# Optimization experiments

Measured on AMD Instinct MI355X. Metric: run time of the kernel, lower is better.

The kernel has to match this reference:

```python
import jax, jax.numpy as jnp
from jax import lax
import numpy as np

N, K, QK, W = 10, 10, 150, 128
D = 256
HID = 100
CHANS = [1, 16, 32, 64, 128, 256]
STRIDES = [2, 2, 1, 1, 1]
ITERS = 3
BN_EPS = 1e-5


def setup_inputs() -> dict:
    key = jax.random.key(0)
    ks = jax.random.split(key, 12)
    inp = {
        "support": jax.random.normal(ks[0], (N, K, 1, W, W), jnp.float32),
        "query": jax.random.normal(ks[1], (QK, 1, W, W), jnp.float32),
    }
    for i in range(5):
        inp[f"conv_w{i}"] = jax.random.normal(ks[2 + i], (CHANS[i + 1], CHANS[i], 3, 3), jnp.float32) * 0.05
        inp[f"bn_g{i}"] = jnp.ones((CHANS[i + 1],), jnp.float32)
        inp[f"bn_b{i}"] = jnp.zeros((CHANS[i + 1],), jnp.float32)
    inp["trans_w"] = jax.random.normal(ks[8], (D, D), jnp.float32) * 0.05
    inp["trans_b"] = jnp.zeros((D,), jnp.float32)
    inp["bil_w"] = jax.random.normal(ks[9], (HID, D, D), jnp.float32) * 0.02
    inp["score_w"] = jax.random.normal(ks[10], (1, HID), jnp.float32) * 0.1
    inp["score_b"] = jnp.zeros((1,), jnp.float32)
    return inp


def _block(x, w, g, b, s):
    # Conv2d(k=3, pad=1, stride=s, no bias) -> BatchNorm(eval: mean=0, var=1) -> ReLU -> MaxPool2d(2)
    x = lax.conv_general_dilated(x, w, (s, s), ((1, 1), (1, 1)),
                                 dimension_numbers=('NCHW', 'OIHW', 'NCHW'))
    scale = (g / jnp.sqrt(1.0 + BN_EPS))[None, :, None, None]
    x = jax.nn.relu(x * scale + b[None, :, None, None])
    return lax.reduce_window(x, -jnp.inf, lax.max, (1, 1, 2, 2), (1, 1, 2, 2), 'VALID')


def reference(support, query,
              conv_w0, conv_w1, conv_w2, conv_w3, conv_w4,
              bn_g0, bn_g1, bn_g2, bn_g3, bn_g4,
              bn_b0, bn_b1, bn_b2, bn_b3, bn_b4,
              trans_w, trans_b, bil_w, score_w, score_b):
    n, k = support.shape[0], support.shape[1]
    qk = query.shape[0]
    w = support.shape[3]

    ws = [conv_w0, conv_w1, conv_w2, conv_w3, conv_w4]
    gs = [bn_g0, bn_g1, bn_g2, bn_g3, bn_g4]
    bs = [bn_b0, bn_b1, bn_b2, bn_b3, bn_b4]

    # run the conv backbone on support+query jointly (BN is per-sample in eval mode)
    x = jnp.concatenate([support.reshape(n * k, 1, w, w), query], axis=0)
    for cw, g, b, s in zip(ws, gs, bs, STRIDES):
        x = _block(x, cw, g, b, s)
    feats = x.reshape(x.shape[0], -1)              # (n*k + qk, 256); spatial is 1x1
    sup = feats[:n * k].reshape(n, k, -1)          # (n, k, d)
    q = feats[n * k:]                              # (qk, d)

    # dynamic routing: Transformer(e) is recomputed each iter on the same input -> hoist
    e = sup @ trans_w.T + trans_b                  # (n, k, d)
    b0 = jnp.zeros((n, k), sup.dtype)

    def step(bb, _):
        dcoef = jax.nn.softmax(bb, axis=1)[:, :, None]   # (n, k, 1)
        c = (dcoef * e).sum(axis=1)                      # (n, d)
        cn = jnp.sqrt((c * c).sum(axis=1, keepdims=True))
        c = c * (cn / (cn * cn + 1.0))                   # squash: ||c||^2/(||c||^2+1)/||c||
        db = (c[:, None, :] * e).sum(axis=2)             # (n, k)
        return bb + db, c

    _, cs = lax.scan(step, b0, None, length=ITERS)
    proto = cs[-1]                                  # (n, d)

    # NTN: bilinear score for every (query, proto) pair, exploiting the pair structure
    t1 = jnp.einsum('nc,hce->nhe', proto, bil_w)    # (n, HID, d)
    v = jnp.einsum('nhe,qe->qnh', t1, q)            # (qk, n, HID)
    s = jax.nn.relu(v) @ score_w[0] + score_b[0]    # (qk, n)
    return jax.nn.log_softmax(s, axis=1)
```

## Files before the change

kernel.cpp:

```cpp
#include <hip/hip_runtime.h>
#include <math.h>


#define BN_SCALE rsqrtf(1.0f + 1e-5f)

#define OFF_A0    0
#define OFF_FEATS 4096000
#define OFF_E     4160000
#define OFF_PROTO 4185600
#define OFF_T1    4188160
#define OFF_W1T   4444160
#define OFF_W2T   4448768
#define OFF_W3T   4467200
#define OFF_W4T   4540928
#define OFF_TWT   4835840

__global__ void k_block0(const float* __restrict__ sup, const float* __restrict__ qry,
                         const float* __restrict__ w0, const float* __restrict__ g0,
                         const float* __restrict__ b0,
                         const float* __restrict__ w1, const float* __restrict__ w2,
                         const float* __restrict__ w3, const float* __restrict__ w4,
                         const float* __restrict__ tw, float* __restrict__ ws) {
  __shared__ float simg[33 * 132];
  float* a0  = ws + OFF_A0;
  float* w1t = ws + OFF_W1T;
  float* w2t = ws + OFF_W2T;
  float* w3t = ws + OFF_W3T;
  float* w4t = ws + OFF_W4T;
  float* twt = ws + OFF_TWT;
  float* t1  = ws + OFF_T1;
  int t = threadIdx.x;
  int task = blockIdx.x;
  int img = task >> 2, band = task & 3;
  const float* in = (img < 100) ? (sup + (size_t)img * 16384)
                                : (qry + (size_t)(img - 100) * 16384);
  int row0 = band * 32 - 1;
  if (t < 33) simg[t * 132] = 0.f;
  for (int i = t; i < 33 * 128; i += 256) {
    int r = i >> 7, cc = i & 127;
    int ry = row0 + r;
    simg[r * 132 + cc + 1] = (ry >= 0) ? in[ry * 128 + cc] : 0.f;
  }
  __syncthreads();
  int lane = t & 63, wid = t >> 6;
  int ox = lane & 31, oyh = lane >> 5;
  int oc0 = wid * 4;
  float wv[36], sc[4], bs[4];
#pragma unroll
  for (int j = 0; j < 4; j++) {
#pragma unroll
    for (int k = 0; k < 9; k++) wv[j * 9 + k] = w0[(oc0 + j) * 9 + k];
    sc[j] = g0[oc0 + j] * BN_SCALE;
    bs[j] = b0[oc0 + j];
  }
#pragma unroll
  for (int oyy = 0; oyy < 4; oyy++) {
    int oy = oyy * 2 + oyh;
    float win[25];
#pragma unroll
    for (int d = 0; d < 5; d++) {
      const float* rp = simg + (4 * oy + d) * 132 + 4 * ox;
      float4 r4 = *(const float4*)rp;
      win[d * 5 + 0] = r4.x; win[d * 5 + 1] = r4.y;
      win[d * 5 + 2] = r4.z; win[d * 5 + 3] = r4.w;
      win[d * 5 + 4] = rp[4];
    }
#pragma unroll
    for (int j = 0; j < 4; j++) {
      float m = -1e30f;
#pragma unroll
      for (int py = 0; py < 2; py++)
#pragma unroll
        for (int px = 0; px < 2; px++) {
          float c = 0.f;
#pragma unroll
          for (int ky = 0; ky < 3; ky++)
#pragma unroll
            for (int kx = 0; kx < 3; kx++)
              c = fmaf(win[(2 * py + ky) * 5 + (2 * px + kx)], wv[j * 9 + ky * 3 + kx], c);
          m = fmaxf(m, fmaf(c, sc[j], bs[j]));
        }
      int OY = band * 8 + oy;
      a0[(((size_t)img * 16 + oc0 + j) * 32 + OY) * 32 + ox] = fmaxf(m, 0.f);
    }
  }
  for (int i = blockIdx.x * 256 + t; i < 713216; i += 256000) {
    if (i < 4608) {
      int oc = i & 31; int r = i >> 5; int tap = r % 9; int ic = r / 9;
      w1t[i] = w1[(oc * 16 + ic) * 9 + tap];
    } else if (i < 23040) {
      int j = i - 4608;
      int oc = j & 63; int r = j >> 6; int tap = r % 9; int ic = r / 9;
      w2t[j] = w2[(oc * 32 + ic) * 9 + tap];
    } else if (i < 96768) {
      int j = i - 23040;
      int oc = j & 127; int r = j >> 7; int tap = r % 9; int ic = r / 9;
      w3t[j] = w3[(oc * 64 + ic) * 9 + tap];
    } else if (i < 391680) {
      int j = i - 96768;
      int oc = j & 255; int r = j >> 8; int tap = r % 9; int ic = r / 9;
      w4t[j] = w4[(oc * 128 + ic) * 9 + tap];
    } else if (i < 457216) {
      int j = i - 391680;
      int d = j >> 8, c = j & 255;
      twt[j] = tw[c * 256 + d];
    } else {
      t1[i - 457216] = 0.f;
    }
  }
}

__global__ void __launch_bounds__(1024, 4)
k_mid(const float* __restrict__ g1, const float* __restrict__ b1,
      const float* __restrict__ g2, const float* __restrict__ b2,
      const float* __restrict__ g3, const float* __restrict__ b3,
      const float* __restrict__ g4, const float* __restrict__ b4,
      const float* __restrict__ tb, float* __restrict__ ws,
      float* __restrict__ feats_g, float* __restrict__ e_buf) {
  __shared__ float S[23424];
  const float* a0  = ws + OFF_A0;
  const float* w1t = ws + OFF_W1T;
  const float* w2t = ws + OFF_W2T;
  const float* w3t = ws + OFF_W3T;
  const float* w4t = ws + OFF_W4T;
  const float* twt = ws + OFF_TWT;
  const int img = blockIdx.x;
  const int t = threadIdx.x;
  float* sa1 = S + 19584;
  float* sa2 = S;
  float* sa3 = S + 4096;
  float* sft = S + 4608;
  float* RED = S + 8192;

  const float* in = a0 + (size_t)img * 16384;
  for (int i = t; i < 19584; i += 1024) {
    int c = i % 36; int r = (i / 36) % 34; int ic = i / 1224;
    int gr = r - 1, gc = c - 1;
    S[i] = (gr >= 0 && gr < 32 && gc >= 0 && gc < 32) ? in[ic * 1024 + gr * 32 + gc] : 0.f;
  }
  for (int i = t; i < 3840; i += 1024) sa1[i] = 0.f;
  __syncthreads();

  {
    int ocp = t & 15;
    int pos = t >> 4;
    int py = pos >> 3, px = pos & 7;
    float acc0[4] = {0.f, 0.f, 0.f, 0.f}, acc1[4] = {0.f, 0.f, 0.f, 0.f};
    for (int ic = 0; ic < 16; ic++) {
      float win[25];
      const float* bp = S + ic * 1224 + 4 * py * 36 + 4 * px;
#pragma unroll
      for (int d = 0; d < 5; d++) {
        float4 r4 = *(const float4*)(bp + d * 36);
        win[d * 5 + 0] = r4.x; win[d * 5 + 1] = r4.y;
        win[d * 5 + 2] = r4.z; win[d * 5 + 3] = r4.w;
        win[d * 5 + 4] = bp[d * 36 + 4];
      }
      float wA[9], wB[9];
#pragma unroll
      for (int k = 0; k < 9; k++) {
        float2 wv = *(const float2*)(w1t + (ic * 9 + k) * 32 + 2 * ocp);
        wA[k] = wv.x; wB[k] = wv.y;
      }
#pragma unroll
      for (int cy = 0; cy < 2; cy++)
#pragma unroll
        for (int cx = 0; cx < 2; cx++) {
          float c0 = acc0[cy * 2 + cx], c1 = acc1[cy * 2 + cx];
#pragma unroll
          for (int ky = 0; ky < 3; ky++)
#pragma unroll
            for (int kx = 0; kx < 3; kx++) {
              float iv = win[(2 * cy + ky) * 5 + (2 * cx + kx)];
              c0 = fmaf(iv, wA[ky * 3 + kx], c0);
              c1 = fmaf(iv, wB[ky * 3 + kx], c1);
            }
          acc0[cy * 2 + cx] = c0; acc1[cy * 2 + cx] = c1;
        }
    }
#pragma unroll
    for (int j = 0; j < 2; j++) {
      int oc = 2 * ocp + j;
      const float* ac = j ? acc1 : acc0;
      float sc = g1[oc] * BN_SCALE, bsj = b1[oc];
      float m = -1e30f;
#pragma unroll
      for (int p = 0; p < 4; p++) m = fmaxf(m, fmaf(ac[p], sc, bsj));
      sa1[oc * 120 + (py + 1) * 12 + (px + 1)] = fmaxf(m, 0.f);
    }
  }
  __syncthreads();
  for (int i = t; i < 3072; i += 1024) sa2[i] = 0.f;
  __syncthreads();

  {
    int oc = t & 63, pos = t >> 6;
    int py = pos >> 2, px = pos & 3;
    float acc[4] = {0.f, 0.f, 0.f, 0.f};
    for (int ic = 0; ic < 32; ic++) {
      float win[16];
      const float* bp = sa1 + ic * 120 + 2 * py * 12 + 2 * px;
#pragma unroll
      for (int r = 0; r < 4; r++) {
        float2 u = *(const float2*)(bp + r * 12);
        float2 v = *(const float2*)(bp + r * 12 + 2);
        win[r * 4 + 0] = u.x; win[r * 4 + 1] = u.y;
        win[r * 4 + 2] = v.x; win[r * 4 + 3] = v.y;
      }
      const float* wp = w2t + ic * 576 + oc;
      float wr[9];
#pragma unroll
      for (int k = 0; k < 9; k++) wr[k] = wp[k * 64];
#pragma unroll
      for (int cy = 0; cy < 2; cy++)
#pragma unroll
        for (int cx = 0; cx < 2; cx++) {
          float c = acc[cy * 2 + cx];
#pragma unroll
          for (int ky = 0; ky < 3; ky++)
#pragma unroll
            for (int kx = 0; kx < 3; kx++)
              c = fmaf(win[(cy + ky) * 4 + (cx + kx)], wr[ky * 3 + kx], c);
          acc[cy * 2 + cx] = c;
        }
    }
    float sc = g2[oc] * BN_SCALE, bsj = b2[oc];
    float m = -1e30f;
#pragma unroll
    for (int p = 0; p < 4; p++) m = fmaxf(m, fmaf(acc[p], sc, bsj));
    sa2[oc * 48 + (py + 1) * 8 + (px + 1)] = fmaxf(m, 0.f);
  }
  __syncthreads();

  {
    int oc = t & 127, pp = (t >> 7) & 3, ich = t >> 9;
    int py = pp >> 1, px = pp & 1;
    float acc[4] = {0.f, 0.f, 0.f, 0.f};
    for (int ii = 0; ii < 32; ii++) {
      int ic = ich * 32 + ii;
      float win[16];
      const float* bp = sa2 + ic * 48 + 2 * py * 8 + 2 * px;
#pragma unroll
      for (int r = 0; r < 4; r++) {
        float2 u = *(const float2*)(bp + r * 8);
        float2 v = *(const float2*)(bp + r * 8 + 2);
        win[r * 4 + 0] = u.x; win[r * 4 + 1] = u.y;
        win[r * 4 + 2] = v.x; win[r * 4 + 3] = v.y;
      }
      const float* wp = w3t + ic * 1152 + oc;
      float wr[9];
#pragma unroll
      for (int k = 0; k < 9; k++) wr[k] = wp[k * 128];
#pragma unroll
      for (int cy = 0; cy < 2; cy++)
#pragma unroll
        for (int cx = 0; cx < 2; cx++) {
          float c = acc[cy * 2 + cx];
#pragma unroll
          for (int ky = 0; ky < 3; ky++)
#pragma unroll
            for (int kx = 0; kx < 3; kx++)
              c = fmaf(win[(cy + ky) * 4 + (cx + kx)], wr[ky * 3 + kx], c);
          acc[cy * 2 + cx] = c;
        }
    }
    if (ich) {
#pragma unroll
      for (int p = 0; p < 4; p++) RED[(t - 512) * 4 + p] = acc[p];
    }
    __syncthreads();
    if (!ich) {
      float sc = g3[oc] * BN_SCALE, bsj = b3[oc];
      float m = -1e30f;
#pragma unroll
      for (int p = 0; p < 4; p++) m = fmaxf(m, fmaf(acc[p] + RED[t * 4 + p], sc, bsj));
      sa3[oc * 4 + pp] = fmaxf(m, 0.f);
    }
  }
  __syncthreads();

  {
    int oc = t & 255, icq = t >> 8;
    float acc[4] = {0.f, 0.f, 0.f, 0.f};
    for (int ii = 0; ii < 32; ii++) {
      int ic = icq * 32 + ii;
      float4 iv = *(const float4*)(sa3 + ic * 4);
      const float* wp = w4t + ic * 2304 + oc;
      float wr[9];
#pragma unroll
      for (int k = 0; k < 9; k++) wr[k] = wp[k * 256];
#pragma unroll
      for (int py = 0; py < 2; py++)
#pragma unroll
        for (int px = 0; px < 2; px++) {
          float c = acc[py * 2 + px];
          c = fmaf(iv.x, wr[(1 - py) * 3 + (1 - px)], c);
          c = fmaf(iv.y, wr[(1 - py) * 3 + (2 - px)], c);
          c = fmaf(iv.z, wr[(2 - py) * 3 + (1 - px)], c);
          c = fmaf(iv.w, wr[(2 - py) * 3 + (2 - px)], c);
          acc[py * 2 + px] = c;
        }
    }
    if (icq) {
#pragma unroll
      for (int p = 0; p < 4; p++) RED[((icq - 1) * 256 + oc) * 4 + p] = acc[p];
    }
    __syncthreads();
    if (icq == 0) {
      float sc = g4[oc] * BN_SCALE, bsj = b4[oc];
      float m = -1e30f;
#pragma unroll
      for (int p = 0; p < 4; p++) {
        float v = acc[p] + RED[oc * 4 + p] + RED[(256 + oc) * 4 + p] + RED[(512 + oc) * 4 + p];
        m = fmaxf(m, fmaf(v, sc, bsj));
      }
      float r = fmaxf(m, 0.f);
      sft[oc] = r;
      feats_g[(size_t)img * 256 + oc] = r;
    }
  }
  __syncthreads();

  if (img < 100) {
    int c = t & 255, dq = t >> 8;
    float acc = 0.f;
#pragma unroll 4
    for (int ii = 0; ii < 64; ii++) {
      int d = dq * 64 + ii;
      acc = fmaf(sft[d], twt[d * 256 + c], acc);
    }
    if (dq) RED[(dq - 1) * 256 + c] = acc;
    __syncthreads();
    if (dq == 0)
      e_buf[img * 256 + c] = acc + RED[c] + RED[256 + c] + RED[512 + c] + tb[c];
  }
}

__global__ void k_routing(const float* __restrict__ e, float* __restrict__ proto) {
  int n = blockIdx.x;
  __shared__ float sb[10], sdc[10], red[4], red2[40], sfc[1];
  int t = threadIdx.x;
  int lane = t & 63, wid = t >> 6;
  float ek[10];
#pragma unroll
  for (int k = 0; k < 10; k++) ek[k] = e[n * 2560 + k * 256 + t];
  if (t < 10) sb[t] = 0.f;
  __syncthreads();
  float cd = 0.f;
  for (int iter = 0; iter < 3; iter++) {
    if (t == 0) {
      float mx = sb[0];
      for (int k = 1; k < 10; k++) mx = fmaxf(mx, sb[k]);
      float sum = 0.f;
      for (int k = 0; k < 10; k++) { float ex = expf(sb[k] - mx); sdc[k] = ex; sum += ex; }
      float inv = 1.f / sum;
      for (int k = 0; k < 10; k++) sdc[k] *= inv;
    }
    __syncthreads();
    cd = 0.f;
#pragma unroll
    for (int k = 0; k < 10; k++) cd = fmaf(sdc[k], ek[k], cd);
    float ss = cd * cd;
#pragma unroll
    for (int off = 32; off > 0; off >>= 1) ss += __shfl_down(ss, off, 64);
    if (lane == 0) red[wid] = ss;
    __syncthreads();
    if (t == 0) {
      float tot = red[0] + red[1] + red[2] + red[3];
      sfc[0] = sqrtf(tot) / (tot + 1.f);
    }
    __syncthreads();
    cd *= sfc[0];
    float pr[10];
#pragma unroll
    for (int k = 0; k < 10; k++) pr[k] = cd * ek[k];
#pragma unroll
    for (int off = 32; off > 0; off >>= 1)
#pragma unroll
      for (int k = 0; k < 10; k++) pr[k] += __shfl_down(pr[k], off, 64);
    if (lane == 0)
#pragma unroll
      for (int k = 0; k < 10; k++) red2[k * 4 + wid] = pr[k];
    __syncthreads();
    if (t < 10) sb[t] += red2[t * 4] + red2[t * 4 + 1] + red2[t * 4 + 2] + red2[t * 4 + 3];
    __syncthreads();
  }
  proto[n * 256 + t] = cd;
}

__global__ void k_t1(const float* __restrict__ proto, const float* __restrict__ bw,
                     float* __restrict__ t1) {
  int b = blockIdx.x;
  int h = b >> 3, c0 = (b & 7) * 32;
  int e = threadIdx.x;
  __shared__ float sp[320];
  for (int i = e; i < 320; i += 256) {
    int n = i >> 5, cl = i & 31;
    sp[i] = proto[n * 256 + c0 + cl];
  }
  __syncthreads();
  float acc[10];
#pragma unroll
  for (int n = 0; n < 10; n++) acc[n] = 0.f;
  const float* wp = bw + ((size_t)h * 256 + c0) * 256 + e;
#pragma unroll 4
  for (int cl = 0; cl < 32; cl++) {
    float wv = wp[(size_t)cl * 256];
#pragma unroll
    for (int n = 0; n < 10; n++) acc[n] = fmaf(sp[n * 32 + cl], wv, acc[n]);
  }
#pragma unroll
  for (int n = 0; n < 10; n++)
    atomicAdd(&t1[((size_t)n * 100 + h) * 256 + e], acc[n]);
}

__global__ void k_score(const float* __restrict__ t1, const float* __restrict__ qf,
                        const float* __restrict__ sw, const float* __restrict__ sbp,
                        float* __restrict__ out) {
  int q = blockIdx.x;
  int t = threadIdx.x, lane = t & 63, wid = t >> 6;
  __shared__ float sred[40];
  float4 qv = *(const float4*)(qf + q * 256 + lane * 4);
  float accn[10];
#pragma unroll
  for (int n = 0; n < 10; n++) accn[n] = 0.f;
  for (int h = wid * 25; h < wid * 25 + 25; h++) {
    float swh = sw[h];
#pragma unroll
    for (int n = 0; n < 10; n++) {
      float4 tv = *(const float4*)(t1 + ((size_t)n * 100 + h) * 256 + lane * 4);
      float pr = tv.x * qv.x + tv.y * qv.y + tv.z * qv.z + tv.w * qv.w;
#pragma unroll
      for (int off = 32; off > 0; off >>= 1) pr += __shfl_down(pr, off, 64);
      if (lane == 0) accn[n] = fmaf(fmaxf(pr, 0.f), swh, accn[n]);
    }
  }
  if (lane == 0)
#pragma unroll
    for (int n = 0; n < 10; n++) sred[wid * 10 + n] = accn[n];
  __syncthreads();
  if (t == 0) {
    float s[10];
    float mx = -1e30f;
    for (int n = 0; n < 10; n++) {
      s[n] = sred[n] + sred[10 + n] + sred[20 + n] + sred[30 + n] + sbp[0];
      mx = fmaxf(mx, s[n]);
    }
    float sum = 0.f;
    for (int n = 0; n < 10; n++) sum += expf(s[n] - mx);
    float lse = mx + logf(sum);
    for (int n = 0; n < 10; n++) out[q * 10 + n] = s[n] - lse;
  }
}

extern "C" void kernel_launch(void* const* d_in, const int* in_sizes, int n_in,
                              void* d_out, int out_size, void* d_ws, size_t ws_size,
                              hipStream_t stream) {
  const float* support = (const float*)d_in[0];
  const float* query   = (const float*)d_in[1];
  const float* conv_w[5]; const float* bn_g[5]; const float* bn_b[5];
  for (int i = 0; i < 5; i++) {
    conv_w[i] = (const float*)d_in[2 + 3 * i];
    bn_g[i]   = (const float*)d_in[3 + 3 * i];
    bn_b[i]   = (const float*)d_in[4 + 3 * i];
  }
  const float* trans_w = (const float*)d_in[17];
  const float* trans_b = (const float*)d_in[18];
  const float* bil_w   = (const float*)d_in[19];
  const float* score_w = (const float*)d_in[20];
  const float* score_b = (const float*)d_in[21];
  float* out = (float*)d_out;
  float* ws = (float*)d_ws;

  float* feats = ws + OFF_FEATS;
  float* e_buf = ws + OFF_E;
  float* proto = ws + OFF_PROTO;
  float* t1    = ws + OFF_T1;

  k_block0<<<1000, 256, 0, stream>>>(support, query, conv_w[0], bn_g[0], bn_b[0],
                                     conv_w[1], conv_w[2], conv_w[3], conv_w[4],
                                     trans_w, ws);
  k_mid<<<250, 1024, 0, stream>>>(bn_g[1], bn_b[1], bn_g[2], bn_b[2],
                                  bn_g[3], bn_b[3], bn_g[4], bn_b[4],
                                  trans_b, ws, feats, e_buf);
  k_routing<<<10, 256, 0, stream>>>(e_buf, proto);
  k_t1<<<800, 256, 0, stream>>>(proto, bil_w, t1);
  k_score<<<150, 256, 0, stream>>>(t1, feats + 100 * 256, score_w, score_b, out);
}
```

Measured before the change: 237.2 us.

## Fuse conv block0 into per-image backbone kernel and merge routing with bilinear

Moves the first conv block into the per-image main kernel, so the 16x32x32 activation stays in shared memory instead of going through global memory, and weight transposes go to a separate small prep kernel. Layers 2 and 3 now give each thread a 4x4 output tile with an input-channel split reduced through shared memory. Routing and the bilinear t1 step are fused into one kernel per hidden unit that recomputes routing redundantly and writes without atomics or a zero-init. Scoring handles three queries per block. The cost is redundant routing work across 100 blocks and more shared-memory pressure with fewer blocks for block0's work.

```diff
diff --git a/kernel.cpp b/kernel.cpp
--- a/kernel.cpp
+++ b/kernel.cpp
@@ -4,121 +4,56 @@
 
 #define BN_SCALE rsqrtf(1.0f + 1e-5f)
 
-#define OFF_A0    0
-#define OFF_FEATS 4096000
-#define OFF_E     4160000
-#define OFF_PROTO 4185600
-#define OFF_T1    4188160
-#define OFF_W1T   4444160
-#define OFF_W2T   4448768
-#define OFF_W3T   4467200
-#define OFF_W4T   4540928
-#define OFF_TWT   4835840
-
-__global__ void k_block0(const float* __restrict__ sup, const float* __restrict__ qry,
-                         const float* __restrict__ w0, const float* __restrict__ g0,
-                         const float* __restrict__ b0,
-                         const float* __restrict__ w1, const float* __restrict__ w2,
-                         const float* __restrict__ w3, const float* __restrict__ w4,
-                         const float* __restrict__ tw, float* __restrict__ ws) {
-  __shared__ float simg[33 * 132];
-  float* a0  = ws + OFF_A0;
+#define OFF_FEATS 0
+#define OFF_E     64000
+#define OFF_T1    89600
+#define OFF_W1T   345600
+#define OFF_W2T   350208
+#define OFF_W3T   368640
+#define OFF_W4T   442368
+#define OFF_TWT   737280
+
+__global__ void k_prep(const float* __restrict__ w1, const float* __restrict__ w2,
+                       const float* __restrict__ w3, const float* __restrict__ w4,
+                       const float* __restrict__ tw, float* __restrict__ ws) {
   float* w1t = ws + OFF_W1T;
   float* w2t = ws + OFF_W2T;
   float* w3t = ws + OFF_W3T;
   float* w4t = ws + OFF_W4T;
   float* twt = ws + OFF_TWT;
-  float* t1  = ws + OFF_T1;
-  int t = threadIdx.x;
-  int task = blockIdx.x;
-  int img = task >> 2, band = task & 3;
-  const float* in = (img < 100) ? (sup + (size_t)img * 16384)
-                                : (qry + (size_t)(img - 100) * 16384);
-  int row0 = band * 32 - 1;
-  if (t < 33) simg[t * 132] = 0.f;
-  for (int i = t; i < 33 * 128; i += 256) {
-    int r = i >> 7, cc = i & 127;
-    int ry = row0 + r;
-    simg[r * 132 + cc + 1] = (ry >= 0) ? in[ry * 128 + cc] : 0.f;
-  }
-  __syncthreads();
-  int lane = t & 63, wid = t >> 6;
-  int ox = lane & 31, oyh = lane >> 5;
-  int oc0 = wid * 4;
-  float wv[36], sc[4], bs[4];
-#pragma unroll
-  for (int j = 0; j < 4; j++) {
-#pragma unroll
-    for (int k = 0; k < 9; k++) wv[j * 9 + k] = w0[(oc0 + j) * 9 + k];
-    sc[j] = g0[oc0 + j] * BN_SCALE;
-    bs[j] = b0[oc0 + j];
-  }
-#pragma unroll
-  for (int oyy = 0; oyy < 4; oyy++) {
-    int oy = oyy * 2 + oyh;
-    float win[25];
-#pragma unroll
-    for (int d = 0; d < 5; d++) {
-      const float* rp = simg + (4 * oy + d) * 132 + 4 * ox;
-      float4 r4 = *(const float4*)rp;
-      win[d * 5 + 0] = r4.x; win[d * 5 + 1] = r4.y;
-      win[d * 5 + 2] = r4.z; win[d * 5 + 3] = r4.w;
-      win[d * 5 + 4] = rp[4];
-    }
-#pragma unroll
-    for (int j = 0; j < 4; j++) {
-      float m = -1e30f;
-#pragma unroll
-      for (int py = 0; py < 2; py++)
-#pragma unroll
-        for (int px = 0; px < 2; px++) {
-          float c = 0.f;
-#pragma unroll
-          for (int ky = 0; ky < 3; ky++)
-#pragma unroll
-            for (int kx = 0; kx < 3; kx++)
-              c = fmaf(win[(2 * py + ky) * 5 + (2 * px + kx)], wv[j * 9 + ky * 3 + kx], c);
-          m = fmaxf(m, fmaf(c, sc[j], bs[j]));
-        }
-      int OY = band * 8 + oy;
-      a0[(((size_t)img * 16 + oc0 + j) * 32 + OY) * 32 + ox] = fmaxf(m, 0.f);
-    }
-  }
-  for (int i = blockIdx.x * 256 + t; i < 713216; i += 256000) {
-    if (i < 4608) {
-      int oc = i & 31; int r = i >> 5; int tap = r % 9; int ic = r / 9;
-      w1t[i] = w1[(oc * 16 + ic) * 9 + tap];
-    } else if (i < 23040) {
-      int j = i - 4608;
-      int oc = j & 63; int r = j >> 6; int tap = r % 9; int ic = r / 9;
-      w2t[j] = w2[(oc * 32 + ic) * 9 + tap];
-    } else if (i < 96768) {
-      int j = i - 23040;
-      int oc = j & 127; int r = j >> 7; int tap = r % 9; int ic = r / 9;
-      w3t[j] = w3[(oc * 64 + ic) * 9 + tap];
-    } else if (i < 391680) {
-      int j = i - 96768;
-      int oc = j & 255; int r = j >> 8; int tap = r % 9; int ic = r / 9;
-      w4t[j] = w4[(oc * 128 + ic) * 9 + tap];
-    } else if (i < 457216) {
-      int j = i - 391680;
-      int d = j >> 8, c = j & 255;
-      twt[j] = tw[c * 256 + d];
-    } else {
-      t1[i - 457216] = 0.f;
-    }
+  int i = blockIdx.x * 256 + threadIdx.x;
+  if (i < 4608) {
+    int oc = i & 31; int r = i >> 5; int tap = r % 9; int ic = r / 9;
+    w1t[i] = w1[(oc * 16 + ic) * 9 + tap];
+  } else if (i < 23040) {
+    int j = i - 4608;
+    int oc = j & 63; int r = j >> 6; int tap = r % 9; int ic = r / 9;
+    w2t[j] = w2[(oc * 32 + ic) * 9 + tap];
+  } else if (i < 96768) {
+    int j = i - 23040;
+    int oc = j & 127; int r = j >> 7; int tap = r % 9; int ic = r / 9;
+    w3t[j] = w3[(oc * 64 + ic) * 9 + tap];
+  } else if (i < 391680) {
+    int j = i - 96768;
+    int oc = j & 255; int r = j >> 8; int tap = r % 9; int ic = r / 9;
+    w4t[j] = w4[(oc * 128 + ic) * 9 + tap];
+  } else {
+    int j = i - 391680;
+    int d = j >> 8, c = j & 255;
+    twt[j] = tw[c * 256 + d];
   }
 }
 
 __global__ void __launch_bounds__(1024, 4)
-k_mid(const float* __restrict__ g1, const float* __restrict__ b1,
-      const float* __restrict__ g2, const float* __restrict__ b2,
-      const float* __restrict__ g3, const float* __restrict__ b3,
-      const float* __restrict__ g4, const float* __restrict__ b4,
-      const float* __restrict__ tb, float* __restrict__ ws,
-      float* __restrict__ feats_g, float* __restrict__ e_buf) {
-  __shared__ float S[23424];
-  const float* a0  = ws + OFF_A0;
+k_main(const float* __restrict__ sup, const float* __restrict__ qry,
+       const float* __restrict__ w0, const float* __restrict__ g0, const float* __restrict__ b0,
+       const float* __restrict__ g1, const float* __restrict__ b1,
+       const float* __restrict__ g2, const float* __restrict__ b2,
+       const float* __restrict__ g3, const float* __restrict__ b3,
+       const float* __restrict__ g4, const float* __restrict__ b4,
+       const float* __restrict__ tb, float* __restrict__ ws,
+       float* __restrict__ feats_g, float* __restrict__ e_buf) {
+  __shared__ float S[28164];
   const float* w1t = ws + OFF_W1T;
   const float* w2t = ws + OFF_W2T;
   const float* w3t = ws + OFF_W3T;
@@ -126,29 +61,77 @@
   const float* twt = ws + OFF_TWT;
   const int img = blockIdx.x;
   const int t = threadIdx.x;
-  float* sa1 = S + 19584;
-  float* sa2 = S;
-  float* sa3 = S + 4096;
-  float* sft = S + 4608;
-  float* RED = S + 8192;
-
-  const float* in = a0 + (size_t)img * 16384;
-  for (int i = t; i < 19584; i += 1024) {
-    int c = i % 36; int r = (i / 36) % 34; int ic = i / 1224;
-    int gr = r - 1, gc = c - 1;
-    S[i] = (gr >= 0 && gr < 32 && gc >= 0 && gc < 32) ? in[ic * 1024 + gr * 32 + gc] : 0.f;
-  }
-  for (int i = t; i < 3840; i += 1024) sa1[i] = 0.f;
-  __syncthreads();
+  const int lane = t & 63, wid = t >> 6;
+  float* a0p = S + 8580;
+  float* sa1 = S;
+  float* sa2 = S + 4096;
+  float* sa3 = S + 7424;
+  float* sft = S + 7936;
+  float* RED = S + 8580;
+
+  const float* in = (img < 100) ? (sup + (size_t)img * 16384)
+                                : (qry + (size_t)(img - 100) * 16384);
 
   {
-    int ocp = t & 15;
-    int pos = t >> 4;
+    int oc = wid;
+    float wv[9];
+#pragma unroll
+    for (int k = 0; k < 9; k++) wv[k] = w0[oc * 9 + k];
+    float sc = g0[oc] * BN_SCALE, bs = b0[oc];
+    int pcol = lane & 31, prh = lane >> 5;
+
+    for (int i = t; i < 19584; i += 1024) a0p[i] = 0.f;
+
+    for (int pass = 0; pass < 2; pass++) {
+      __syncthreads();
+      for (int i = t; i < 8580; i += 1024) {
+        int r = i / 132, c = i % 132;
+        int ir = pass ? (63 + r) : (r - 1);
+        int icl = c - 1;
+        S[i] = (ir >= 0 && ir < 128 && icl >= 0 && icl < 128) ? in[ir * 128 + icl] : 0.f;
+      }
+      __syncthreads();
+#pragma unroll
+      for (int it = 0; it < 8; it++) {
+        int prl = it * 2 + prh;
+        float win[25];
+#pragma unroll
+        for (int d = 0; d < 5; d++) {
+          const float* rp = S + (4 * prl + d) * 132 + 4 * pcol;
+          float4 r4 = *(const float4*)rp;
+          win[d * 5 + 0] = r4.x; win[d * 5 + 1] = r4.y;
+          win[d * 5 + 2] = r4.z; win[d * 5 + 3] = r4.w;
+          win[d * 5 + 4] = rp[4];
+        }
+        float m = -1e30f;
+#pragma unroll
+        for (int a = 0; a < 2; a++)
+#pragma unroll
+          for (int b = 0; b < 2; b++) {
+            float c = 0.f;
+#pragma unroll
+            for (int ky = 0; ky < 3; ky++)
+#pragma unroll
+              for (int kx = 0; kx < 3; kx++)
+                c = fmaf(win[(2 * a + ky) * 5 + (2 * b + kx)], wv[ky * 3 + kx], c);
+            m = fmaxf(m, fmaf(c, sc, bs));
+          }
+        int PR = pass * 16 + prl;
+        a0p[oc * 1224 + (PR + 1) * 36 + (pcol + 1)] = fmaxf(m, 0.f);
+      }
+    }
+  }
+  __syncthreads();
+  for (int i = t; i < 7424; i += 1024) S[i] = 0.f;
+  __syncthreads();
+
+  {
+    int ocp = t & 15, pos = t >> 4;
     int py = pos >> 3, px = pos & 7;
     float acc0[4] = {0.f, 0.f, 0.f, 0.f}, acc1[4] = {0.f, 0.f, 0.f, 0.f};
     for (int ic = 0; ic < 16; ic++) {
       float win[25];
-      const float* bp = S + ic * 1224 + 4 * py * 36 + 4 * px;
+      const float* bp = a0p + ic * 1224 + 4 * py * 36 + 4 * px;
 #pragma unroll
       for (int d = 0; d < 5; d++) {
         float4 r4 = *(const float4*)(bp + d * 36);
@@ -186,96 +169,125 @@
       float m = -1e30f;
 #pragma unroll
       for (int p = 0; p < 4; p++) m = fmaxf(m, fmaf(ac[p], sc, bsj));
-      sa1[oc * 120 + (py + 1) * 12 + (px + 1)] = fmaxf(m, 0.f);
-    }
-  }
-  __syncthreads();
-  for (int i = t; i < 3072; i += 1024) sa2[i] = 0.f;
+      sa1[oc * 124 + (py + 1) * 12 + (px + 1)] = fmaxf(m, 0.f);
+    }
+  }
   __syncthreads();
 
   {
-    int oc = t & 63, pos = t >> 6;
-    int py = pos >> 2, px = pos & 3;
-    float acc[4] = {0.f, 0.f, 0.f, 0.f};
-    for (int ic = 0; ic < 32; ic++) {
-      float win[16];
-      const float* bp = sa1 + ic * 120 + 2 * py * 12 + 2 * px;
-#pragma unroll
-      for (int r = 0; r < 4; r++) {
-        float2 u = *(const float2*)(bp + r * 12);
-        float2 v = *(const float2*)(bp + r * 12 + 2);
-        win[r * 4 + 0] = u.x; win[r * 4 + 1] = u.y;
-        win[r * 4 + 2] = v.x; win[r * 4 + 3] = v.y;
+    int oc = t & 63, icg = (t >> 6) & 3, pg = t >> 8;
+    int pgy = pg >> 1, pgx = pg & 1;
+    float acc[16];
+#pragma unroll
+    for (int p = 0; p < 16; p++) acc[p] = 0.f;
+    for (int ii = 0; ii < 8; ii++) {
+      int ic = icg * 8 + ii;
+      float win[6][6];
+      const float* bp = sa1 + ic * 124 + 4 * pgy * 12 + 4 * pgx;
+#pragma unroll
+      for (int d = 0; d < 6; d++) {
+        float4 u = *(const float4*)(bp + d * 12);
+        float2 v = *(const float2*)(bp + d * 12 + 4);
+        win[d][0] = u.x; win[d][1] = u.y; win[d][2] = u.z; win[d][3] = u.w;
+        win[d][4] = v.x; win[d][5] = v.y;
       }
       const float* wp = w2t + ic * 576 + oc;
       float wr[9];
 #pragma unroll
       for (int k = 0; k < 9; k++) wr[k] = wp[k * 64];
 #pragma unroll
-      for (int cy = 0; cy < 2; cy++)
-#pragma unroll
-        for (int cx = 0; cx < 2; cx++) {
-          float c = acc[cy * 2 + cx];
+      for (int u = 0; u < 4; u++)
+#pragma unroll
+        for (int v = 0; v < 4; v++) {
+          float c = acc[u * 4 + v];
 #pragma unroll
           for (int ky = 0; ky < 3; ky++)
 #pragma unroll
             for (int kx = 0; kx < 3; kx++)
-              c = fmaf(win[(cy + ky) * 4 + (cx + kx)], wr[ky * 3 + kx], c);
-          acc[cy * 2 + cx] = c;
+              c = fmaf(win[u + ky][v + kx], wr[ky * 3 + kx], c);
+          acc[u * 4 + v] = c;
         }
     }
+#pragma unroll
+    for (int j = 0; j < 16; j++) RED[j * 1024 + icg * 256 + pg * 64 + oc] = acc[j];
+  }
+  __syncthreads();
+  if (t < 256) {
+    int oc = t & 63, pg = t >> 6;
+    int pgy = pg >> 1, pgx = pg & 1;
     float sc = g2[oc] * BN_SCALE, bsj = b2[oc];
-    float m = -1e30f;
-#pragma unroll
-    for (int p = 0; p < 4; p++) m = fmaxf(m, fmaf(acc[p], sc, bsj));
-    sa2[oc * 48 + (py + 1) * 8 + (px + 1)] = fmaxf(m, 0.f);
+#pragma unroll
+    for (int cy = 0; cy < 2; cy++)
+#pragma unroll
+      for (int cx = 0; cx < 2; cx++) {
+        float m = -1e30f;
+#pragma unroll
+        for (int a = 0; a < 2; a++)
+#pragma unroll
+          for (int b = 0; b < 2; b++) {
+            int j = (2 * cy + a) * 4 + (2 * cx + b);
+            float v = RED[j * 1024 + pg * 64 + oc] + RED[j * 1024 + 256 + pg * 64 + oc]
+                    + RED[j * 1024 + 512 + pg * 64 + oc] + RED[j * 1024 + 768 + pg * 64 + oc];
+            m = fmaxf(m, fmaf(v, sc, bsj));
+          }
+        sa2[oc * 52 + (1 + 2 * pgy + cy) * 8 + (1 + 2 * pgx + cx)] = fmaxf(m, 0.f);
+      }
   }
   __syncthreads();
 
   {
-    int oc = t & 127, pp = (t >> 7) & 3, ich = t >> 9;
-    int py = pp >> 1, px = pp & 1;
-    float acc[4] = {0.f, 0.f, 0.f, 0.f};
-    for (int ii = 0; ii < 32; ii++) {
-      int ic = ich * 32 + ii;
-      float win[16];
-      const float* bp = sa2 + ic * 48 + 2 * py * 8 + 2 * px;
-#pragma unroll
-      for (int r = 0; r < 4; r++) {
-        float2 u = *(const float2*)(bp + r * 8);
-        float2 v = *(const float2*)(bp + r * 8 + 2);
-        win[r * 4 + 0] = u.x; win[r * 4 + 1] = u.y;
-        win[r * 4 + 2] = v.x; win[r * 4 + 3] = v.y;
+    int oc = t & 127, icg = t >> 7;
+    float acc[16];
+#pragma unroll
+    for (int p = 0; p < 16; p++) acc[p] = 0.f;
+    for (int ii = 0; ii < 8; ii++) {
+      int ic = icg * 8 + ii;
+      float win[6][6];
+      const float* bp = sa2 + ic * 52;
+#pragma unroll
+      for (int d = 0; d < 6; d++) {
+        float4 u = *(const float4*)(bp + d * 8);
+        float2 v = *(const float2*)(bp + d * 8 + 4);
+        win[d][0] = u.x; win[d][1] = u.y; win[d][2] = u.z; win[d][3] = u.w;
+        win[d][4] = v.x; win[d][5] = v.y;
       }
       const float* wp = w3t + ic * 1152 + oc;
       float wr[9];
 #pragma unroll
       for (int k = 0; k < 9; k++) wr[k] = wp[k * 128];
 #pragma unroll
-      for (int cy = 0; cy < 2; cy++)
-#pragma unroll
-        for (int cx = 0; cx < 2; cx++) {
-          float c = acc[cy * 2 + cx];
+      for (int u = 0; u < 4; u++)
+#pragma unroll
+        for (int v = 0; v < 4; v++) {
+          float c = acc[u * 4 + v];
 #pragma unroll
           for (int ky = 0; ky < 3; ky++)
 #pragma unroll
             for (int kx = 0; kx < 3; kx++)
-              c = fmaf(win[(cy + ky) * 4 + (cx + kx)], wr[ky * 3 + kx], c);
-          acc[cy * 2 + cx] = c;
+              c = fmaf(win[u + ky][v + kx], wr[ky * 3 + kx], c);
+          acc[u * 4 + v] = c;
         }
     }
-    if (ich) {
-#pragma unroll
-      for (int p = 0; p < 4; p++) RED[(t - 512) * 4 + p] = acc[p];
-    }
-    __syncthreads();
-    if (!ich) {
-      float sc = g3[oc] * BN_SCALE, bsj = b3[oc];
-      float m = -1e30f;
-#pragma unroll
-      for (int p = 0; p < 4; p++) m = fmaxf(m, fmaf(acc[p] + RED[t * 4 + p], sc, bsj));
-      sa3[oc * 4 + pp] = fmaxf(m, 0.f);
-    }
+#pragma unroll
+    for (int j = 0; j < 16; j++) RED[j * 1024 + icg * 128 + oc] = acc[j];
+  }
+  __syncthreads();
+  if (t < 512) {
+    int oc = t & 127, pp = t >> 7;
+    int py = pp >> 1, px = pp & 1;
+    float sc = g3[oc] * BN_SCALE, bsj = b3[oc];
+    float m = -1e30f;
+#pragma unroll
+    for (int a = 0; a < 2; a++)
+#pragma unroll
+      for (int b = 0; b < 2; b++) {
+        int j = (2 * py + a) * 4 + (2 * px + b);
+        float v = 0.f;
+#pragma unroll
+        for (int g = 0; g < 8; g++) v += RED[j * 1024 + g * 128 + oc];
+        m = fmaxf(m, fmaf(v, sc, bsj));
+      }
+    sa3[oc * 4 + pp] = fmaxf(m, 0.f);
   }
   __syncthreads();
 
@@ -336,120 +348,127 @@
   }
 }
 
-__global__ void k_routing(const float* __restrict__ e, float* __restrict__ proto) {
-  int n = blockIdx.x;
-  __shared__ float sb[10], sdc[10], red[4], red2[40], sfc[1];
-  int t = threadIdx.x;
-  int lane = t & 63, wid = t >> 6;
-  float ek[10];
-#pragma unroll
-  for (int k = 0; k < 10; k++) ek[k] = e[n * 2560 + k * 256 + t];
-  if (t < 10) sb[t] = 0.f;
-  __syncthreads();
-  float cd = 0.f;
-  for (int iter = 0; iter < 3; iter++) {
-    if (t == 0) {
-      float mx = sb[0];
-      for (int k = 1; k < 10; k++) mx = fmaxf(mx, sb[k]);
-      float sum = 0.f;
-      for (int k = 0; k < 10; k++) { float ex = expf(sb[k] - mx); sdc[k] = ex; sum += ex; }
+__global__ void k_rt1(const float* __restrict__ e, const float* __restrict__ bw,
+                      float* __restrict__ t1) {
+  __shared__ float pt[3072];
+  __shared__ float red[4], red2[40];
+  const int h = blockIdx.x;
+  const int t = threadIdx.x, lane = t & 63, wid = t >> 6;
+
+  for (int n = 0; n < 10; n++) {
+    float ek[10];
+#pragma unroll
+    for (int k = 0; k < 10; k++) ek[k] = e[n * 2560 + k * 256 + t];
+    float b[10];
+#pragma unroll
+    for (int k = 0; k < 10; k++) b[k] = 0.f;
+    float cd = 0.f;
+    for (int iter = 0; iter < 3; iter++) {
+      float mx = b[0];
+#pragma unroll
+      for (int k = 1; k < 10; k++) mx = fmaxf(mx, b[k]);
+      float sdc[10], sum = 0.f;
+#pragma unroll
+      for (int k = 0; k < 10; k++) { sdc[k] = expf(b[k] - mx); sum += sdc[k]; }
       float inv = 1.f / sum;
-      for (int k = 0; k < 10; k++) sdc[k] *= inv;
-    }
-    __syncthreads();
-    cd = 0.f;
-#pragma unroll
-    for (int k = 0; k < 10; k++) cd = fmaf(sdc[k], ek[k], cd);
-    float ss = cd * cd;
-#pragma unroll
-    for (int off = 32; off > 0; off >>= 1) ss += __shfl_down(ss, off, 64);
-    if (lane == 0) red[wid] = ss;
-    __syncthreads();
-    if (t == 0) {
+      cd = 0.f;
+#pragma unroll
+      for (int k = 0; k < 10; k++) cd = fmaf(sdc[k] * inv, ek[k], cd);
+      float ss = cd * cd;
+#pragma unroll
+      for (int off = 32; off > 0; off >>= 1) ss += __shfl_down(ss, off, 64);
+      if (lane == 0) red[wid] = ss;
+      __syncthreads();
       float tot = red[0] + red[1] + red[2] + red[3];
-      sfc[0] = sqrtf(tot) / (tot + 1.f);
-    }
-    __syncthreads();
-    cd *= sfc[0];
-    float pr[10];
-#pragma unroll
-    for (int k = 0; k < 10; k++) pr[k] = cd * ek[k];
-#pragma unroll
-    for (int off = 32; off > 0; off >>= 1)
-#pragma unroll
-      for (int k = 0; k < 10; k++) pr[k] += __shfl_down(pr[k], off, 64);
-    if (lane == 0)
-#pragma unroll
-      for (int k = 0; k < 10; k++) red2[k * 4 + wid] = pr[k];
-    __syncthreads();
-    if (t < 10) sb[t] += red2[t * 4] + red2[t * 4 + 1] + red2[t * 4 + 2] + red2[t * 4 + 3];
-    __syncthreads();
-  }
-  proto[n * 256 + t] = cd;
-}
-
-__global__ void k_t1(const float* __restrict__ proto, const float* __restrict__ bw,
-                     float* __restrict__ t1) {
-  int b = blockIdx.x;
-  int h = b >> 3, c0 = (b & 7) * 32;
-  int e = threadIdx.x;
-  __shared__ float sp[320];
-  for (int i = e; i < 320; i += 256) {
-    int n = i >> 5, cl = i & 31;
-    sp[i] = proto[n * 256 + c0 + cl];
-  }
-  __syncthreads();
+      cd *= sqrtf(tot) / (tot + 1.f);
+      float pr[10];
+#pragma unroll
+      for (int k = 0; k < 10; k++) pr[k] = cd * ek[k];
+#pragma unroll
+      for (int off = 32; off > 0; off >>= 1)
+#pragma unroll
+        for (int k = 0; k < 10; k++) pr[k] += __shfl_down(pr[k], off, 64);
+      if (lane == 0)
+#pragma unroll
+        for (int k = 0; k < 10; k++) red2[k * 4 + wid] = pr[k];
+      __syncthreads();
+#pragma unroll
+      for (int k = 0; k < 10; k++)
+        b[k] += red2[k * 4] + red2[k * 4 + 1] + red2[k * 4 + 2] + red2[k * 4 + 3];
+      __syncthreads();
+    }
+    pt[t * 12 + n] = cd;
+  }
+  __syncthreads();
+
   float acc[10];
 #pragma unroll
   for (int n = 0; n < 10; n++) acc[n] = 0.f;
-  const float* wp = bw + ((size_t)h * 256 + c0) * 256 + e;
-#pragma unroll 4
-  for (int cl = 0; cl < 32; cl++) {
-    float wv = wp[(size_t)cl * 256];
-#pragma unroll
-    for (int n = 0; n < 10; n++) acc[n] = fmaf(sp[n * 32 + cl], wv, acc[n]);
-  }
-#pragma unroll
-  for (int n = 0; n < 10; n++)
-    atomicAdd(&t1[((size_t)n * 100 + h) * 256 + e], acc[n]);
+  const float* wp = bw + (size_t)h * 65536 + t;
+#pragma unroll 2
+  for (int c = 0; c < 256; c++) {
+    float wv = wp[(size_t)c * 256];
+    float4 p0 = *(const float4*)(pt + c * 12);
+    float4 p1 = *(const float4*)(pt + c * 12 + 4);
+    float2 p2 = *(const float2*)(pt + c * 12 + 8);
+    acc[0] = fmaf(p0.x, wv, acc[0]); acc[1] = fmaf(p0.y, wv, acc[1]);
+    acc[2] = fmaf(p0.z, wv, acc[2]); acc[3] = fmaf(p0.w, wv, acc[3]);
+    acc[4] = fmaf(p1.x, wv, acc[4]); acc[5] = fmaf(p1.y, wv, acc[5]);
+    acc[6] = fmaf(p1.z, wv, acc[6]); acc[7] = fmaf(p1.w, wv, acc[7]);
+    acc[8] = fmaf(p2.x, wv, acc[8]); acc[9] = fmaf(p2.y, wv, acc[9]);
+  }
+#pragma unroll
+  for (int n = 0; n < 10; n++) t1[((size_t)n * 100 + h) * 256 + t] = acc[n];
 }
 
 __global__ void k_score(const float* __restrict__ t1, const float* __restrict__ qf,
                         const float* __restrict__ sw, const float* __restrict__ sbp,
                         float* __restrict__ out) {
-  int q = blockIdx.x;
-  int t = threadIdx.x, lane = t & 63, wid = t >> 6;
-  __shared__ float sred[40];
-  float4 qv = *(const float4*)(qf + q * 256 + lane * 4);
-  float accn[10];
-#pragma unroll
-  for (int n = 0; n < 10; n++) accn[n] = 0.f;
+  __shared__ float sred[4][30];
+  __shared__ float ssc[30];
+  const int q0 = blockIdx.x * 3;
+  const int t = threadIdx.x, lane = t & 63, wid = t >> 6;
+  float4 qv[3];
+#pragma unroll
+  for (int j = 0; j < 3; j++) qv[j] = *(const float4*)(qf + (q0 + j) * 256 + lane * 4);
+  float accn[3][10];
+#pragma unroll
+  for (int j = 0; j < 3; j++)
+#pragma unroll
+    for (int n = 0; n < 10; n++) accn[j][n] = 0.f;
   for (int h = wid * 25; h < wid * 25 + 25; h++) {
     float swh = sw[h];
 #pragma unroll
     for (int n = 0; n < 10; n++) {
       float4 tv = *(const float4*)(t1 + ((size_t)n * 100 + h) * 256 + lane * 4);
-      float pr = tv.x * qv.x + tv.y * qv.y + tv.z * qv.z + tv.w * qv.w;
-#pragma unroll
-      for (int off = 32; off > 0; off >>= 1) pr += __shfl_down(pr, off, 64);
-      if (lane == 0) accn[n] = fmaf(fmaxf(pr, 0.f), swh, accn[n]);
+      float pr[3];
+#pragma unroll
+      for (int j = 0; j < 3; j++)
+        pr[j] = tv.x * qv[j].x + tv.y * qv[j].y + tv.z * qv[j].z + tv.w * qv[j].w;
+#pragma unroll
+      for (int off = 32; off > 0; off >>= 1)
+#pragma unroll
+        for (int j = 0; j < 3; j++) pr[j] += __shfl_down(pr[j], off, 64);
+      if (lane == 0)
+#pragma unroll
+        for (int j = 0; j < 3; j++) accn[j][n] = fmaf(fmaxf(pr[j], 0.f), swh, accn[j][n]);
     }
   }
   if (lane == 0)
 #pragma unroll
-    for (int n = 0; n < 10; n++) sred[wid * 10 + n] = accn[n];
-  __syncthreads();
-  if (t == 0) {
-    float s[10];
+    for (int j = 0; j < 3; j++)
+#pragma unroll
+      for (int n = 0; n < 10; n++) sred[wid][j * 10 + n] = accn[j][n];
+  __syncthreads();
+  if (t < 30) ssc[t] = sred[0][t] + sred[1][t] + sred[2][t] + sred[3][t] + sbp[0];
+  __syncthreads();
+  if (t < 3) {
     float mx = -1e30f;
-    for (int n = 0; n < 10; n++) {
-      s[n] = sred[n] + sred[10 + n] + sred[20 + n] + sred[30 + n] + sbp[0];
-      mx = fmaxf(mx, s[n]);
-    }
+    for (int n = 0; n < 10; n++) mx = fmaxf(mx, ssc[t * 10 + n]);
     float sum = 0.f;
-    for (int n = 0; n < 10; n++) sum += expf(s[n] - mx);
+    for (int n = 0; n < 10; n++) sum += expf(ssc[t * 10 + n] - mx);
     float lse = mx + logf(sum);
-    for (int n = 0; n < 10; n++) out[q * 10 + n] = s[n] - lse;
+    for (int n = 0; n < 10; n++) out[(q0 + t) * 10 + n] = ssc[t * 10 + n] - lse;
   }
 }
 
@@ -474,16 +493,15 @@
 
   float* feats = ws + OFF_FEATS;
   float* e_buf = ws + OFF_E;
-  float* proto = ws + OFF_PROTO;
   float* t1    = ws + OFF_T1;
 
-  k_block0<<<1000, 256, 0, stream>>>(support, query, conv_w[0], bn_g[0], bn_b[0],
-                                     conv_w[1], conv_w[2], conv_w[3], conv_w[4],
-                                     trans_w, ws);
-  k_mid<<<250, 1024, 0, stream>>>(bn_g[1], bn_b[1], bn_g[2], bn_b[2],
-                                  bn_g[3], bn_b[3], bn_g[4], bn_b[4],
-                                  trans_b, ws, feats, e_buf);
-  k_routing<<<10, 256, 0, stream>>>(e_buf, proto);
-  k_t1<<<800, 256, 0, stream>>>(proto, bil_w, t1);
-  k_score<<<150, 256, 0, stream>>>(t1, feats + 100 * 256, score_w, score_b, out);
+  k_prep<<<1786, 256, 0, stream>>>(conv_w[1], conv_w[2], conv_w[3], conv_w[4],
+                                   trans_w, ws);
+  k_main<<<250, 1024, 0, stream>>>(support, query,
+                                   conv_w[0], bn_g[0], bn_b[0],
+                                   bn_g[1], bn_b[1], bn_g[2], bn_b[2],
+                                   bn_g[3], bn_b[3], bn_g[4], bn_b[4],
+                                   trans_b, ws, feats, e_buf);
+  k_rt1<<<100, 256, 0, stream>>>(e_buf, bil_w, t1);
+  k_score<<<50, 256, 0, stream>>>(t1, feats + 100 * 256, score_w, score_b, out);
 }
```

Measured after the change: 395.8 us. 1.67x slower.
